# Kernel optimization log

Hardware: AMD Instinct MI355X
Metric: run time of the kernel (lower is better)

## Reference

```python
import jax, jax.numpy as jnp
import numpy as np

N = 100000
E = 1600000
IN_CH = 128
EDGE_CH = 16
HID = 128
OUT = 4
EPS = 1e-12  # F.normalize eps


def l2_normalize(x):
    # matches torch.nn.functional.normalize(x, p=2, dim=1)
    norm = jnp.sqrt(jnp.sum(x * x, axis=1, keepdims=True))
    return x / jnp.maximum(norm, EPS)


def sage_conv(x, row, col, edge_attr, W, b, n_nodes):
    # gather source node feats, concat edge feats: [E, in+edge]
    m = jnp.concatenate([x[row], edge_attr], axis=1)
    m = l2_normalize(m)
    # scatter-mean by destination node
    s = jax.ops.segment_sum(m, col, num_segments=n_nodes)
    cnt = jax.ops.segment_sum(jnp.ones((m.shape[0],), m.dtype), col, num_segments=n_nodes)
    agg = s / jnp.maximum(cnt, 1.0)[:, None]
    out = agg @ W + b
    return l2_normalize(out)


def setup_inputs() -> dict:
    key = jax.random.key(0)
    ks = jax.random.split(key, 7)
    x = jax.random.normal(ks[0], (N, IN_CH), dtype=jnp.float32)
    edge_index = jax.random.randint(ks[1], (2, E), 0, N, dtype=jnp.int64)
    edge_attr = jax.random.normal(ks[2], (E, EDGE_CH), dtype=jnp.float32)
    W1 = jax.random.normal(ks[3], (IN_CH + EDGE_CH, HID), dtype=jnp.float32) / np.sqrt(IN_CH + EDGE_CH)
    b1 = jnp.zeros((HID,), dtype=jnp.float32)
    W2 = jax.random.normal(ks[4], (HID + EDGE_CH, OUT), dtype=jnp.float32) / np.sqrt(HID + EDGE_CH)
    b2 = jnp.zeros((OUT,), dtype=jnp.float32)
    return {"x": x, "edge_index": edge_index, "edge_attr": edge_attr,
            "W1": W1, "b1": b1, "W2": W2, "b2": b2}


def reference(x, edge_index, edge_attr, W1, b1, W2, b2):
    row, col = edge_index[0], edge_index[1]
    h = sage_conv(x, row, col, edge_attr, W1, b1, N)
    h = jax.nn.relu(h)  # dropout is identity in eval mode
    h = sage_conv(h, row, col, edge_attr, W2, b2, N)
    return jax.nn.sigmoid(h)
```

## Files before the change

### kernel.cpp

```cpp
#include <hip/hip_runtime.h>
#include <hip/hip_fp16.h>
#include <math.h>

#define N_NODES 100000
#define N_EDGES 1600000
#define CHUNK 1024
#define NCHUNKS ((N_NODES + CHUNK - 1) / CHUNK)

union H8 { uint4 u; __half2 h[4]; };

__device__ __forceinline__ float red32(float v) {
    #pragma unroll
    for (int m = 16; m >= 1; m >>= 1) v += __shfl_xor(v, m, 64);
    return v;
}

__global__ __launch_bounds__(256) void prep_edges(
        const float* __restrict__ ea, const int* __restrict__ col,
        const float* __restrict__ W2,
        float* __restrict__ sqea, float4* __restrict__ pea,
        __half* __restrict__ eah, int* __restrict__ cnt) {
    __shared__ float w2e[64];
    int t = threadIdx.x;
    if (t < 64) w2e[t] = W2[128 * 4 + t];
    __syncthreads();
    int e = blockIdx.x * 256 + t;
    if (e >= N_EDGES) return;
    const float4* p = (const float4*)(ea + (size_t)e * 16);
    float4 q0 = p[0], q1 = p[1], q2 = p[2], q3 = p[3];
    float a[16] = {q0.x,q0.y,q0.z,q0.w, q1.x,q1.y,q1.z,q1.w,
                   q2.x,q2.y,q2.z,q2.w, q3.x,q3.y,q3.z,q3.w};
    float s = 0.f;
    float4 pv = make_float4(0.f, 0.f, 0.f, 0.f);
    #pragma unroll
    for (int k = 0; k < 16; ++k) {
        s += a[k] * a[k];
        pv.x += a[k] * w2e[k * 4 + 0];
        pv.y += a[k] * w2e[k * 4 + 1];
        pv.z += a[k] * w2e[k * 4 + 2];
        pv.w += a[k] * w2e[k * 4 + 3];
    }
    sqea[e] = s;
    pea[e] = pv;
    H8 u0, u1;
    u0.h[0] = __float22half2_rn(make_float2(q0.x, q0.y));
    u0.h[1] = __float22half2_rn(make_float2(q0.z, q0.w));
    u0.h[2] = __float22half2_rn(make_float2(q1.x, q1.y));
    u0.h[3] = __float22half2_rn(make_float2(q1.z, q1.w));
    u1.h[0] = __float22half2_rn(make_float2(q2.x, q2.y));
    u1.h[1] = __float22half2_rn(make_float2(q2.z, q2.w));
    u1.h[2] = __float22half2_rn(make_float2(q3.x, q3.y));
    u1.h[3] = __float22half2_rn(make_float2(q3.z, q3.w));
    uint4* dst = (uint4*)(eah + (size_t)e * 16);
    dst[0] = u0.u; dst[1] = u1.u;
    atomicAdd(&cnt[col[e]], 1);
}

__global__ void scan_part(const int* __restrict__ cnt, int* __restrict__ psum) {
    __shared__ int sd[CHUNK];
    int i = blockIdx.x * CHUNK + threadIdx.x;
    sd[threadIdx.x] = (i < N_NODES) ? cnt[i] : 0;
    __syncthreads();
    for (int s = CHUNK / 2; s > 0; s >>= 1) {
        if (threadIdx.x < s) sd[threadIdx.x] += sd[threadIdx.x + s];
        __syncthreads();
    }
    if (threadIdx.x == 0) psum[blockIdx.x] = sd[0];
}

__global__ void scan_top(const int* __restrict__ psum, int* __restrict__ coff,
                         int* __restrict__ off) {
    if (blockIdx.x == 0 && threadIdx.x == 0) {
        int run = 0;
        for (int i = 0; i < NCHUNKS; ++i) { coff[i] = run; run += psum[i]; }
        off[N_NODES] = N_EDGES;
    }
}

__global__ void scan_apply(const int* __restrict__ cnt, const int* __restrict__ coff,
                           int* __restrict__ off, int* __restrict__ head) {
    __shared__ int sd[CHUNK];
    int i = blockIdx.x * CHUNK + threadIdx.x;
    int v = (i < N_NODES) ? cnt[i] : 0;
    sd[threadIdx.x] = v;
    __syncthreads();
    for (int s = 1; s < CHUNK; s <<= 1) {
        int t = (threadIdx.x >= s) ? sd[threadIdx.x - s] : 0;
        __syncthreads();
        sd[threadIdx.x] += t;
        __syncthreads();
    }
    if (i < N_NODES) {
        int excl = coff[blockIdx.x] + sd[threadIdx.x] - v;
        off[i] = excl;
        head[i] = excl;
    }
}

__global__ __launch_bounds__(256) void scatter_e(
        const int* __restrict__ row, const int* __restrict__ col,
        const float* __restrict__ nx, const float* __restrict__ sqea,
        int* __restrict__ head, int4* __restrict__ csr4, int* __restrict__ epos) {
    int e = blockIdx.x * blockDim.x + threadIdx.x;
    if (e >= N_EDGES) return;
    int c = col[e];
    int r = row[e];
    float w1 = rsqrtf(fmaxf(nx[r] + sqea[e], 1e-24f));
    int p = atomicAdd(&head[c], 1);
    int4 mt; mt.x = r; mt.y = __float_as_int(w1); mt.z = e; mt.w = 0;
    csr4[p] = mt;
    epos[e] = p;
}

__global__ __launch_bounds__(256) void gemm_y1h(const float* __restrict__ x,
                                                const float* __restrict__ W1,
                                                __half* __restrict__ y1h,
                                                float* __restrict__ nx) {
    __shared__ float xs[64][129];
    int r0 = blockIdx.x * 64;
    int t = threadIdx.x;
    for (int i = t; i < 64 * 32; i += 256) {
        int rr = i >> 5, c4 = (i & 31) * 4;
        int gr = r0 + rr;
        float4 v = (gr < N_NODES) ? *(const float4*)(x + (size_t)gr * 128 + c4)
                                  : make_float4(0.f, 0.f, 0.f, 0.f);
        xs[rr][c4] = v.x; xs[rr][c4 + 1] = v.y; xs[rr][c4 + 2] = v.z; xs[rr][c4 + 3] = v.w;
    }
    __syncthreads();
    {
        int rr = t >> 2, q = t & 3;
        float s = 0.f;
        #pragma unroll
        for (int k = 0; k < 32; ++k) { float v = xs[rr][q * 32 + k]; s += v * v; }
        s += __shfl_xor(s, 1, 64);
        s += __shfl_xor(s, 2, 64);
        if (q == 0 && r0 + rr < N_NODES) nx[r0 + rr] = s;
    }
    int tx = t & 31, ty = t >> 5;
    float4 acc[8];
    #pragma unroll
    for (int i = 0; i < 8; ++i) acc[i] = make_float4(0.f, 0.f, 0.f, 0.f);
    #pragma unroll 4
    for (int k = 0; k < 128; ++k) {
        float4 wv = *(const float4*)(W1 + (size_t)k * 128 + tx * 4);
        #pragma unroll
        for (int i = 0; i < 8; ++i) {
            float xv = xs[ty * 8 + i][k];
            acc[i].x += xv * wv.x; acc[i].y += xv * wv.y;
            acc[i].z += xv * wv.z; acc[i].w += xv * wv.w;
        }
    }
    #pragma unroll
    for (int i = 0; i < 8; ++i) {
        int rr = r0 + ty * 8 + i;
        if (rr < N_NODES) {
            H8 pk;
            pk.h[0] = __float22half2_rn(make_float2(acc[i].x, acc[i].y));
            pk.h[1] = __float22half2_rn(make_float2(acc[i].z, acc[i].w));
            *(uint2*)(y1h + (size_t)rr * 128 + tx * 4) = make_uint2(pk.u.x, pk.u.y);
        }
    }
}

__global__ __launch_bounds__(256) void layer1(
        const __half* __restrict__ y1h, const __half* __restrict__ eah,
        const int4* __restrict__ csr4, const int* __restrict__ off,
        const float* __restrict__ W1, const float* __restrict__ b1,
        const float* __restrict__ W2, float* __restrict__ hn) {
    __shared__ int4  smeta[4][64];
    __shared__ float strans[4][144];
    int wv = threadIdx.x >> 6;
    int node = (blockIdx.x << 2) | wv;
    int lane = threadIdx.x & 63;
    if (node >= N_NODES) return;
    int s = off[node], e = off[node + 1];
    int deg = e - s;
    int m = (deg < 64) ? deg : 64;
    if (lane < m) smeta[wv][lane] = csr4[s + lane];
    asm volatile("s_waitcnt lgkmcnt(0)" ::: "memory");

    int e4 = lane >> 4;
    int c8 = lane & 15;
    float4 a0 = make_float4(0,0,0,0), a1 = a0;
    float4 ae0 = a0, ae1 = a0;

    #pragma unroll 2
    for (int t = 0; t < m; t += 4) {
        int idx = t + e4;
        bool val = idx < m;
        int4 mt = smeta[wv][val ? idx : 0];
        float w = val ? __int_as_float(mt.y) : 0.f;
        H8 pk; pk.u = *(const uint4*)(y1h + (size_t)mt.x * 128 + c8 * 8);
        float2 f0 = __half22float2(pk.h[0]);
        float2 f1 = __half22float2(pk.h[1]);
        float2 f2 = __half22float2(pk.h[2]);
        float2 f3 = __half22float2(pk.h[3]);
        a0.x += f0.x * w; a0.y += f0.y * w; a0.z += f1.x * w; a0.w += f1.y * w;
        a1.x += f2.x * w; a1.y += f2.y * w; a1.z += f3.x * w; a1.w += f3.y * w;
        if (c8 < 2) {
            H8 ek; ek.u = *(const uint4*)(eah + (size_t)mt.z * 16 + c8 * 8);
            float2 g0 = __half22float2(ek.h[0]);
            float2 g1 = __half22float2(ek.h[1]);
            float2 g2 = __half22float2(ek.h[2]);
            float2 g3 = __half22float2(ek.h[3]);
            ae0.x += g0.x * w; ae0.y += g0.y * w; ae0.z += g1.x * w; ae0.w += g1.y * w;
            ae1.x += g2.x * w; ae1.y += g2.y * w; ae1.z += g3.x * w; ae1.w += g3.y * w;
        }
    }
    for (int t = 64 + e4; t < deg; t += 4) {
        int4 mt = csr4[s + t];
        float w = __int_as_float(mt.y);
        H8 pk; pk.u = *(const uint4*)(y1h + (size_t)mt.x * 128 + c8 * 8);
        float2 f0 = __half22float2(pk.h[0]);
        float2 f1 = __half22float2(pk.h[1]);
        float2 f2 = __half22float2(pk.h[2]);
        float2 f3 = __half22float2(pk.h[3]);
        a0.x += f0.x * w; a0.y += f0.y * w; a0.z += f1.x * w; a0.w += f1.y * w;
        a1.x += f2.x * w; a1.y += f2.y * w; a1.z += f3.x * w; a1.w += f3.y * w;
        if (c8 < 2) {
            H8 ek; ek.u = *(const uint4*)(eah + (size_t)mt.z * 16 + c8 * 8);
            float2 g0 = __half22float2(ek.h[0]);
            float2 g1 = __half22float2(ek.h[1]);
            float2 g2 = __half22float2(ek.h[2]);
            float2 g3 = __half22float2(ek.h[3]);
            ae0.x += g0.x * w; ae0.y += g0.y * w; ae0.z += g1.x * w; ae0.w += g1.y * w;
            ae1.x += g2.x * w; ae1.y += g2.y * w; ae1.z += g3.x * w; ae1.w += g3.y * w;
        }
    }
    #pragma unroll
    for (int mm = 16; mm <= 32; mm <<= 1) {
        a0.x += __shfl_xor(a0.x, mm, 64); a0.y += __shfl_xor(a0.y, mm, 64);
        a0.z += __shfl_xor(a0.z, mm, 64); a0.w += __shfl_xor(a0.w, mm, 64);
        a1.x += __shfl_xor(a1.x, mm, 64); a1.y += __shfl_xor(a1.y, mm, 64);
        a1.z += __shfl_xor(a1.z, mm, 64); a1.w += __shfl_xor(a1.w, mm, 64);
        ae0.x += __shfl_xor(ae0.x, mm, 64); ae0.y += __shfl_xor(ae0.y, mm, 64);
        ae0.z += __shfl_xor(ae0.z, mm, 64); ae0.w += __shfl_xor(ae0.w, mm, 64);
        ae1.x += __shfl_xor(ae1.x, mm, 64); ae1.y += __shfl_xor(ae1.y, mm, 64);
        ae1.z += __shfl_xor(ae1.z, mm, 64); ae1.w += __shfl_xor(ae1.w, mm, 64);
    }
    if (e4 == 0) {
        *(float4*)&strans[wv][c8 * 8]     = a0;
        *(float4*)&strans[wv][c8 * 8 + 4] = a1;
        if (c8 < 2) {
            *(float4*)&strans[wv][128 + c8 * 8]     = ae0;
            *(float4*)&strans[wv][128 + c8 * 8 + 4] = ae1;
        }
    }
    asm volatile("s_waitcnt lgkmcnt(0)" ::: "memory");

    int c = lane & 31;
    float ic = 1.0f / fmaxf((float)deg, 1.0f);
    float4 av = *(const float4*)&strans[wv][c * 4];
    float4 b1v = *(const float4*)(b1 + c * 4);
    float4 o;
    o.x = av.x * ic + b1v.x; o.y = av.y * ic + b1v.y;
    o.z = av.z * ic + b1v.z; o.w = av.w * ic + b1v.w;
    #pragma unroll
    for (int k = 0; k < 16; ++k) {
        float sk = strans[wv][128 + k] * ic;
        float4 wv4 = *((const float4*)(W1 + (size_t)(128 + k) * 128) + c);
        o.x += sk * wv4.x; o.y += sk * wv4.y; o.z += sk * wv4.z; o.w += sk * wv4.w;
    }
    float ss    = o.x*o.x + o.y*o.y + o.z*o.z + o.w*o.w;
    float sspos = (o.x > 0.f ? o.x*o.x : 0.f) + (o.y > 0.f ? o.y*o.y : 0.f)
                + (o.z > 0.f ? o.z*o.z : 0.f) + (o.w > 0.f ? o.w*o.w : 0.f);
    ss = red32(ss);
    sspos = red32(sspos);
    float inv = rsqrtf(fmaxf(ss, 1e-24f));
    float4 h4;
    h4.x = fmaxf(o.x * inv, 0.f); h4.y = fmaxf(o.y * inv, 0.f);
    h4.z = fmaxf(o.z * inv, 0.f); h4.w = fmaxf(o.w * inv, 0.f);
    float nhv = sspos * inv * inv;
    float4 w0 = *(const float4*)(W2 + (size_t)(4*c + 0) * 4);
    float4 w1 = *(const float4*)(W2 + (size_t)(4*c + 1) * 4);
    float4 w2 = *(const float4*)(W2 + (size_t)(4*c + 2) * 4);
    float4 w3 = *(const float4*)(W2 + (size_t)(4*c + 3) * 4);
    float4 p;
    p.x = h4.x*w0.x + h4.y*w1.x + h4.z*w2.x + h4.w*w3.x;
    p.y = h4.x*w0.y + h4.y*w1.y + h4.z*w2.y + h4.w*w3.y;
    p.z = h4.x*w0.z + h4.y*w1.z + h4.z*w2.z + h4.w*w3.z;
    p.w = h4.x*w0.w + h4.y*w1.w + h4.z*w2.w + h4.w*w3.w;
    p.x = red32(p.x); p.y = red32(p.y); p.z = red32(p.z); p.w = red32(p.w);
    if (lane == 0) {
        *(float4*)(hn + (size_t)node * 8) = p;
        hn[(size_t)node * 8 + 4] = nhv;
    }
}

__global__ __launch_bounds__(256) void cpass(
        const int* __restrict__ row, const float* __restrict__ hn,
        const float* __restrict__ sqea, const float4* __restrict__ pea,
        const int* __restrict__ epos, float4* __restrict__ cbuf) {
    int e = blockIdx.x * blockDim.x + threadIdx.x;
    if (e >= N_EDGES) return;
    int r = row[e];
    float4 yh4 = *(const float4*)(hn + (size_t)r * 8);
    float nhr = hn[(size_t)r * 8 + 4];
    float w2 = rsqrtf(fmaxf(nhr + sqea[e], 1e-24f));
    float4 pe = pea[e];
    float4 cv;
    cv.x = (yh4.x + pe.x) * w2; cv.y = (yh4.y + pe.y) * w2;
    cv.z = (yh4.z + pe.z) * w2; cv.w = (yh4.w + pe.w) * w2;
    cbuf[epos[e]] = cv;
}

__global__ __launch_bounds__(256) void layer2b(
        const float4* __restrict__ cbuf, const int* __restrict__ off,
        const float* __restrict__ b2, float* __restrict__ out) {
    int v = blockIdx.x * blockDim.x + threadIdx.x;
    if (v >= N_NODES) return;
    int s = off[v], e = off[v + 1];
    float4 a = make_float4(0.f, 0.f, 0.f, 0.f);
    for (int t = s; t < e; ++t) {
        float4 cv = cbuf[t];
        a.x += cv.x; a.y += cv.y; a.z += cv.z; a.w += cv.w;
    }
    float ic = 1.0f / fmaxf((float)(e - s), 1.0f);
    float4 o;
    o.x = a.x * ic + b2[0]; o.y = a.y * ic + b2[1];
    o.z = a.z * ic + b2[2]; o.w = a.w * ic + b2[3];
    float ss = o.x*o.x + o.y*o.y + o.z*o.z + o.w*o.w;
    float inv = rsqrtf(fmaxf(ss, 1e-24f));
    float4 res;
    res.x = 1.0f / (1.0f + expf(-(o.x * inv)));
    res.y = 1.0f / (1.0f + expf(-(o.y * inv)));
    res.z = 1.0f / (1.0f + expf(-(o.z * inv)));
    res.w = 1.0f / (1.0f + expf(-(o.w * inv)));
    *(float4*)(out + (size_t)v * 4) = res;
}

extern "C" void kernel_launch(void* const* d_in, const int* in_sizes, int n_in,
                              void* d_out, int out_size, void* d_ws, size_t ws_size,
                              hipStream_t stream) {
    const float* x   = (const float*)d_in[0];
    const int*   ei  = (const int*)d_in[1];
    const float* ea  = (const float*)d_in[2];
    const float* W1  = (const float*)d_in[3];
    const float* b1  = (const float*)d_in[4];
    const float* W2  = (const float*)d_in[5];
    const float* b2  = (const float*)d_in[6];
    const int* row = ei;
    const int* col = ei + N_EDGES;
    float* out = (float*)d_out;

    char* ws = (char*)d_ws;
    size_t o = 0;
    auto carve = [&](size_t bytes) { char* p = ws + o; o = (o + bytes + 255) & ~(size_t)255; return p; };
    __half* y1h    = (__half*)carve((size_t)N_NODES * 128 * 2);
    float4* cbuf   = (float4*)y1h;
    float*  sqea   = (float*)carve((size_t)N_EDGES * 4);
    int4*   csr4   = (int4*)carve((size_t)N_EDGES * 16);
    int*    epos   = (int*)carve((size_t)N_EDGES * 4);
    float4* pea    = (float4*)carve((size_t)N_EDGES * 16);
    __half* eah    = (__half*)carve((size_t)N_EDGES * 16 * 2);
    int*    cnt    = (int*)carve((size_t)N_NODES * 4);
    int*    off    = (int*)carve((size_t)(N_NODES + 1) * 4);
    int*    head   = (int*)carve((size_t)N_NODES * 4);
    float*  nx     = (float*)carve((size_t)N_NODES * 4);
    float*  hn     = (float*)carve((size_t)N_NODES * 8 * 4);
    int*    psum   = (int*)carve((size_t)NCHUNKS * 4);
    int*    coff   = (int*)carve((size_t)NCHUNKS * 4);
    (void)ws_size; (void)in_sizes; (void)n_in; (void)out_size;

    hipMemsetAsync(cnt, 0, (size_t)N_NODES * 4, stream);

    dim3 b256(256);
    prep_edges<<<(N_EDGES + 255) / 256, b256, 0, stream>>>(ea, col, W2, sqea, pea, eah, cnt);
    gemm_y1h<<<(N_NODES + 63) / 64, b256, 0, stream>>>(x, W1, y1h, nx);

    scan_part<<<NCHUNKS, CHUNK, 0, stream>>>(cnt, psum);
    scan_top<<<1, 64, 0, stream>>>(psum, coff, off);
    scan_apply<<<NCHUNKS, CHUNK, 0, stream>>>(cnt, coff, off, head);
    scatter_e<<<(N_EDGES + 255) / 256, b256, 0, stream>>>(row, col, nx, sqea, head,
                                                          csr4, epos);

    layer1<<<(N_NODES + 3) / 4, b256, 0, stream>>>(y1h, eah, csr4, off, W1, b1, W2, hn);
    cpass<<<(N_EDGES + 255) / 256, b256, 0, stream>>>(row, hn, sqea, pea, epos, cbuf);
    layer2b<<<(N_NODES + 255) / 256, b256, 0, stream>>>(cbuf, off, b2, out);
}
```

Measured before the change: 427.8 us.

## Store edge data in CSR order and fuse layer-2 edge pass into node gather

Splits the histogram out of edge prep, then fuses edge preprocessing into the scatter kernel so that edge-feature halves, edge projections and squared norms are written directly at their CSR slot. Layer 1 then reads edge features contiguously instead of through an edge-id indirection, and the CSR metadata shrinks from 16 to 8 bytes. The separate cpass and layer2b kernels are replaced by a single wave-per-node layer2 kernel that computes each edge contribution and reduces it with shuffles, removing the cbuf round trip and the epos array. The cost is scattered writes of larger per-edge payloads during scatter_e, and one wave per node in layer2 leaves most lanes idle when degree is low.

```diff
diff --git a/kernel.cpp b/kernel.cpp
--- a/kernel.cpp
+++ b/kernel.cpp
@@ -15,11 +15,60 @@
     return v;
 }
 
-__global__ __launch_bounds__(256) void prep_edges(
-        const float* __restrict__ ea, const int* __restrict__ col,
-        const float* __restrict__ W2,
-        float* __restrict__ sqea, float4* __restrict__ pea,
-        __half* __restrict__ eah, int* __restrict__ cnt) {
+__global__ __launch_bounds__(256) void hist(const int* __restrict__ col,
+                                            int* __restrict__ cnt) {
+    int e = blockIdx.x * blockDim.x + threadIdx.x;
+    if (e >= N_EDGES) return;
+    atomicAdd(&cnt[col[e]], 1);
+}
+
+__global__ void scan_part(const int* __restrict__ cnt, int* __restrict__ psum) {
+    __shared__ int sd[CHUNK];
+    int i = blockIdx.x * CHUNK + threadIdx.x;
+    sd[threadIdx.x] = (i < N_NODES) ? cnt[i] : 0;
+    __syncthreads();
+    for (int s = CHUNK / 2; s > 0; s >>= 1) {
+        if (threadIdx.x < s) sd[threadIdx.x] += sd[threadIdx.x + s];
+        __syncthreads();
+    }
+    if (threadIdx.x == 0) psum[blockIdx.x] = sd[0];
+}
+
+__global__ void scan_top(const int* __restrict__ psum, int* __restrict__ coff,
+                         int* __restrict__ off) {
+    if (blockIdx.x == 0 && threadIdx.x == 0) {
+        int run = 0;
+        for (int i = 0; i < NCHUNKS; ++i) { coff[i] = run; run += psum[i]; }
+        off[N_NODES] = N_EDGES;
+    }
+}
+
+__global__ void scan_apply(const int* __restrict__ cnt, const int* __restrict__ coff,
+                           int* __restrict__ off, int* __restrict__ head) {
+    __shared__ int sd[CHUNK];
+    int i = blockIdx.x * CHUNK + threadIdx.x;
+    int v = (i < N_NODES) ? cnt[i] : 0;
+    sd[threadIdx.x] = v;
+    __syncthreads();
+    for (int s = 1; s < CHUNK; s <<= 1) {
+        int t = (threadIdx.x >= s) ? sd[threadIdx.x - s] : 0;
+        __syncthreads();
+        sd[threadIdx.x] += t;
+        __syncthreads();
+    }
+    if (i < N_NODES) {
+        int excl = coff[blockIdx.x] + sd[threadIdx.x] - v;
+        off[i] = excl;
+        head[i] = excl;
+    }
+}
+
+__global__ __launch_bounds__(256) void scatter_e(
+        const int* __restrict__ row, const int* __restrict__ col,
+        const float* __restrict__ nx, const float* __restrict__ ea,
+        const float* __restrict__ W2, int* __restrict__ head,
+        float2* __restrict__ csrA, float2* __restrict__ csrB,
+        float4* __restrict__ peaC, __half* __restrict__ eahC) {
     __shared__ float w2e[64];
     int t = threadIdx.x;
     if (t < 64) w2e[t] = W2[128 * 4 + t];
@@ -40,8 +89,13 @@
         pv.z += a[k] * w2e[k * 4 + 2];
         pv.w += a[k] * w2e[k * 4 + 3];
     }
-    sqea[e] = s;
-    pea[e] = pv;
+    int r = row[e];
+    int c = col[e];
+    float w1 = rsqrtf(fmaxf(nx[r] + s, 1e-24f));
+    int pp = atomicAdd(&head[c], 1);
+    csrA[pp] = make_float2(__int_as_float(r), w1);
+    csrB[pp] = make_float2(__int_as_float(r), s);
+    peaC[pp] = pv;
     H8 u0, u1;
     u0.h[0] = __float22half2_rn(make_float2(q0.x, q0.y));
     u0.h[1] = __float22half2_rn(make_float2(q0.z, q0.w));
@@ -51,65 +105,8 @@
     u1.h[1] = __float22half2_rn(make_float2(q2.z, q2.w));
     u1.h[2] = __float22half2_rn(make_float2(q3.x, q3.y));
     u1.h[3] = __float22half2_rn(make_float2(q3.z, q3.w));
-    uint4* dst = (uint4*)(eah + (size_t)e * 16);
+    uint4* dst = (uint4*)(eahC + (size_t)pp * 16);
     dst[0] = u0.u; dst[1] = u1.u;
-    atomicAdd(&cnt[col[e]], 1);
-}
-
-__global__ void scan_part(const int* __restrict__ cnt, int* __restrict__ psum) {
-    __shared__ int sd[CHUNK];
-    int i = blockIdx.x * CHUNK + threadIdx.x;
-    sd[threadIdx.x] = (i < N_NODES) ? cnt[i] : 0;
-    __syncthreads();
-    for (int s = CHUNK / 2; s > 0; s >>= 1) {
-        if (threadIdx.x < s) sd[threadIdx.x] += sd[threadIdx.x + s];
-        __syncthreads();
-    }
-    if (threadIdx.x == 0) psum[blockIdx.x] = sd[0];
-}
-
-__global__ void scan_top(const int* __restrict__ psum, int* __restrict__ coff,
-                         int* __restrict__ off) {
-    if (blockIdx.x == 0 && threadIdx.x == 0) {
-        int run = 0;
-        for (int i = 0; i < NCHUNKS; ++i) { coff[i] = run; run += psum[i]; }
-        off[N_NODES] = N_EDGES;
-    }
-}
-
-__global__ void scan_apply(const int* __restrict__ cnt, const int* __restrict__ coff,
-                           int* __restrict__ off, int* __restrict__ head) {
-    __shared__ int sd[CHUNK];
-    int i = blockIdx.x * CHUNK + threadIdx.x;
-    int v = (i < N_NODES) ? cnt[i] : 0;
-    sd[threadIdx.x] = v;
-    __syncthreads();
-    for (int s = 1; s < CHUNK; s <<= 1) {
-        int t = (threadIdx.x >= s) ? sd[threadIdx.x - s] : 0;
-        __syncthreads();
-        sd[threadIdx.x] += t;
-        __syncthreads();
-    }
-    if (i < N_NODES) {
-        int excl = coff[blockIdx.x] + sd[threadIdx.x] - v;
-        off[i] = excl;
-        head[i] = excl;
-    }
-}
-
-__global__ __launch_bounds__(256) void scatter_e(
-        const int* __restrict__ row, const int* __restrict__ col,
-        const float* __restrict__ nx, const float* __restrict__ sqea,
-        int* __restrict__ head, int4* __restrict__ csr4, int* __restrict__ epos) {
-    int e = blockIdx.x * blockDim.x + threadIdx.x;
-    if (e >= N_EDGES) return;
-    int c = col[e];
-    int r = row[e];
-    float w1 = rsqrtf(fmaxf(nx[r] + sqea[e], 1e-24f));
-    int p = atomicAdd(&head[c], 1);
-    int4 mt; mt.x = r; mt.y = __float_as_int(w1); mt.z = e; mt.w = 0;
-    csr4[p] = mt;
-    epos[e] = p;
 }
 
 __global__ __launch_bounds__(256) void gemm_y1h(const float* __restrict__ x,
@@ -163,11 +160,11 @@
 }
 
 __global__ __launch_bounds__(256) void layer1(
-        const __half* __restrict__ y1h, const __half* __restrict__ eah,
-        const int4* __restrict__ csr4, const int* __restrict__ off,
+        const __half* __restrict__ y1h, const __half* __restrict__ eahC,
+        const float2* __restrict__ csrA, const int* __restrict__ off,
         const float* __restrict__ W1, const float* __restrict__ b1,
         const float* __restrict__ W2, float* __restrict__ hn) {
-    __shared__ int4  smeta[4][64];
+    __shared__ float2 smeta[4][64];
     __shared__ float strans[4][144];
     int wv = threadIdx.x >> 6;
     int node = (blockIdx.x << 2) | wv;
@@ -176,7 +173,7 @@
     int s = off[node], e = off[node + 1];
     int deg = e - s;
     int m = (deg < 64) ? deg : 64;
-    if (lane < m) smeta[wv][lane] = csr4[s + lane];
+    if (lane < m) smeta[wv][lane] = csrA[s + lane];
     asm volatile("s_waitcnt lgkmcnt(0)" ::: "memory");
 
     int e4 = lane >> 4;
@@ -188,9 +185,10 @@
     for (int t = 0; t < m; t += 4) {
         int idx = t + e4;
         bool val = idx < m;
-        int4 mt = smeta[wv][val ? idx : 0];
-        float w = val ? __int_as_float(mt.y) : 0.f;
-        H8 pk; pk.u = *(const uint4*)(y1h + (size_t)mt.x * 128 + c8 * 8);
+        float2 mt = smeta[wv][val ? idx : 0];
+        int r = __float_as_int(mt.x);
+        float w = val ? mt.y : 0.f;
+        H8 pk; pk.u = *(const uint4*)(y1h + (size_t)r * 128 + c8 * 8);
         float2 f0 = __half22float2(pk.h[0]);
         float2 f1 = __half22float2(pk.h[1]);
         float2 f2 = __half22float2(pk.h[2]);
@@ -198,7 +196,7 @@
         a0.x += f0.x * w; a0.y += f0.y * w; a0.z += f1.x * w; a0.w += f1.y * w;
         a1.x += f2.x * w; a1.y += f2.y * w; a1.z += f3.x * w; a1.w += f3.y * w;
         if (c8 < 2) {
-            H8 ek; ek.u = *(const uint4*)(eah + (size_t)mt.z * 16 + c8 * 8);
+            H8 ek; ek.u = *(const uint4*)(eahC + (size_t)(s + idx) * 16 + c8 * 8);
             float2 g0 = __half22float2(ek.h[0]);
             float2 g1 = __half22float2(ek.h[1]);
             float2 g2 = __half22float2(ek.h[2]);
@@ -208,9 +206,10 @@
         }
     }
     for (int t = 64 + e4; t < deg; t += 4) {
-        int4 mt = csr4[s + t];
-        float w = __int_as_float(mt.y);
-        H8 pk; pk.u = *(const uint4*)(y1h + (size_t)mt.x * 128 + c8 * 8);
+        float2 mt = csrA[s + t];
+        int r = __float_as_int(mt.x);
+        float w = mt.y;
+        H8 pk; pk.u = *(const uint4*)(y1h + (size_t)r * 128 + c8 * 8);
         float2 f0 = __half22float2(pk.h[0]);
         float2 f1 = __half22float2(pk.h[1]);
         float2 f2 = __half22float2(pk.h[2]);
@@ -218,7 +217,7 @@
         a0.x += f0.x * w; a0.y += f0.y * w; a0.z += f1.x * w; a0.w += f1.y * w;
         a1.x += f2.x * w; a1.y += f2.y * w; a1.z += f3.x * w; a1.w += f3.y * w;
         if (c8 < 2) {
-            H8 ek; ek.u = *(const uint4*)(eah + (size_t)mt.z * 16 + c8 * 8);
+            H8 ek; ek.u = *(const uint4*)(eahC + (size_t)(s + t) * 16 + c8 * 8);
             float2 g0 = __half22float2(ek.h[0]);
             float2 g1 = __half22float2(ek.h[1]);
             float2 g2 = __half22float2(ek.h[2]);
@@ -287,46 +286,49 @@
     }
 }
 
-__global__ __launch_bounds__(256) void cpass(
-        const int* __restrict__ row, const float* __restrict__ hn,
-        const float* __restrict__ sqea, const float4* __restrict__ pea,
-        const int* __restrict__ epos, float4* __restrict__ cbuf) {
-    int e = blockIdx.x * blockDim.x + threadIdx.x;
-    if (e >= N_EDGES) return;
-    int r = row[e];
-    float4 yh4 = *(const float4*)(hn + (size_t)r * 8);
-    float nhr = hn[(size_t)r * 8 + 4];
-    float w2 = rsqrtf(fmaxf(nhr + sqea[e], 1e-24f));
-    float4 pe = pea[e];
-    float4 cv;
-    cv.x = (yh4.x + pe.x) * w2; cv.y = (yh4.y + pe.y) * w2;
-    cv.z = (yh4.z + pe.z) * w2; cv.w = (yh4.w + pe.w) * w2;
-    cbuf[epos[e]] = cv;
-}
-
-__global__ __launch_bounds__(256) void layer2b(
-        const float4* __restrict__ cbuf, const int* __restrict__ off,
+__global__ __launch_bounds__(256) void layer2(
+        const float2* __restrict__ csrB, const float4* __restrict__ peaC,
+        const float* __restrict__ hn, const int* __restrict__ off,
         const float* __restrict__ b2, float* __restrict__ out) {
-    int v = blockIdx.x * blockDim.x + threadIdx.x;
-    if (v >= N_NODES) return;
-    int s = off[v], e = off[v + 1];
-    float4 a = make_float4(0.f, 0.f, 0.f, 0.f);
-    for (int t = s; t < e; ++t) {
-        float4 cv = cbuf[t];
-        a.x += cv.x; a.y += cv.y; a.z += cv.z; a.w += cv.w;
-    }
-    float ic = 1.0f / fmaxf((float)(e - s), 1.0f);
-    float4 o;
-    o.x = a.x * ic + b2[0]; o.y = a.y * ic + b2[1];
-    o.z = a.z * ic + b2[2]; o.w = a.w * ic + b2[3];
-    float ss = o.x*o.x + o.y*o.y + o.z*o.z + o.w*o.w;
-    float inv = rsqrtf(fmaxf(ss, 1e-24f));
-    float4 res;
-    res.x = 1.0f / (1.0f + expf(-(o.x * inv)));
-    res.y = 1.0f / (1.0f + expf(-(o.y * inv)));
-    res.z = 1.0f / (1.0f + expf(-(o.z * inv)));
-    res.w = 1.0f / (1.0f + expf(-(o.w * inv)));
-    *(float4*)(out + (size_t)v * 4) = res;
+    int wv = threadIdx.x >> 6;
+    int node = (blockIdx.x << 2) | wv;
+    int lane = threadIdx.x & 63;
+    if (node >= N_NODES) return;
+    int s = off[node], e = off[node + 1];
+    int deg = e - s;
+    float4 acc = make_float4(0.f, 0.f, 0.f, 0.f);
+    for (int t = lane; t < deg; t += 64) {
+        float2 mb = csrB[s + t];
+        int r = __float_as_int(mb.x);
+        float sq = mb.y;
+        float4 yh = *(const float4*)(hn + (size_t)r * 8);
+        float nh = hn[(size_t)r * 8 + 4];
+        float w = rsqrtf(fmaxf(nh + sq, 1e-24f));
+        float4 pe = peaC[s + t];
+        acc.x += (yh.x + pe.x) * w; acc.y += (yh.y + pe.y) * w;
+        acc.z += (yh.z + pe.z) * w; acc.w += (yh.w + pe.w) * w;
+    }
+    #pragma unroll
+    for (int mm = 32; mm >= 1; mm >>= 1) {
+        acc.x += __shfl_xor(acc.x, mm, 64);
+        acc.y += __shfl_xor(acc.y, mm, 64);
+        acc.z += __shfl_xor(acc.z, mm, 64);
+        acc.w += __shfl_xor(acc.w, mm, 64);
+    }
+    if (lane == 0) {
+        float ic = 1.0f / fmaxf((float)deg, 1.0f);
+        float4 o;
+        o.x = acc.x * ic + b2[0]; o.y = acc.y * ic + b2[1];
+        o.z = acc.z * ic + b2[2]; o.w = acc.w * ic + b2[3];
+        float ss = o.x*o.x + o.y*o.y + o.z*o.z + o.w*o.w;
+        float inv = rsqrtf(fmaxf(ss, 1e-24f));
+        float4 res;
+        res.x = 1.0f / (1.0f + expf(-(o.x * inv)));
+        res.y = 1.0f / (1.0f + expf(-(o.y * inv)));
+        res.z = 1.0f / (1.0f + expf(-(o.z * inv)));
+        res.w = 1.0f / (1.0f + expf(-(o.w * inv)));
+        *(float4*)(out + (size_t)node * 4) = res;
+    }
 }
 
 extern "C" void kernel_launch(void* const* d_in, const int* in_sizes, int n_in,
@@ -347,12 +349,10 @@
     size_t o = 0;
     auto carve = [&](size_t bytes) { char* p = ws + o; o = (o + bytes + 255) & ~(size_t)255; return p; };
     __half* y1h    = (__half*)carve((size_t)N_NODES * 128 * 2);
-    float4* cbuf   = (float4*)y1h;
-    float*  sqea   = (float*)carve((size_t)N_EDGES * 4);
-    int4*   csr4   = (int4*)carve((size_t)N_EDGES * 16);
-    int*    epos   = (int*)carve((size_t)N_EDGES * 4);
-    float4* pea    = (float4*)carve((size_t)N_EDGES * 16);
-    __half* eah    = (__half*)carve((size_t)N_EDGES * 16 * 2);
+    float2* csrA   = (float2*)carve((size_t)N_EDGES * 8);
+    float2* csrB   = (float2*)carve((size_t)N_EDGES * 8);
+    float4* peaC   = (float4*)carve((size_t)N_EDGES * 16);
+    __half* eahC   = (__half*)carve((size_t)N_EDGES * 16 * 2);
     int*    cnt    = (int*)carve((size_t)N_NODES * 4);
     int*    off    = (int*)carve((size_t)(N_NODES + 1) * 4);
     int*    head   = (int*)carve((size_t)N_NODES * 4);
@@ -365,16 +365,15 @@
     hipMemsetAsync(cnt, 0, (size_t)N_NODES * 4, stream);
 
     dim3 b256(256);
-    prep_edges<<<(N_EDGES + 255) / 256, b256, 0, stream>>>(ea, col, W2, sqea, pea, eah, cnt);
+    hist<<<(N_EDGES + 255) / 256, b256, 0, stream>>>(col, cnt);
     gemm_y1h<<<(N_NODES + 63) / 64, b256, 0, stream>>>(x, W1, y1h, nx);
 
     scan_part<<<NCHUNKS, CHUNK, 0, stream>>>(cnt, psum);
     scan_top<<<1, 64, 0, stream>>>(psum, coff, off);
     scan_apply<<<NCHUNKS, CHUNK, 0, stream>>>(cnt, coff, off, head);
-    scatter_e<<<(N_EDGES + 255) / 256, b256, 0, stream>>>(row, col, nx, sqea, head,
-                                                          csr4, epos);
-
-    layer1<<<(N_NODES + 3) / 4, b256, 0, stream>>>(y1h, eah, csr4, off, W1, b1, W2, hn);
-    cpass<<<(N_EDGES + 255) / 256, b256, 0, stream>>>(row, hn, sqea, pea, epos, cbuf);
-    layer2b<<<(N_NODES + 255) / 256, b256, 0, stream>>>(cbuf, off, b2, out);
-}
+    scatter_e<<<(N_EDGES + 255) / 256, b256, 0, stream>>>(row, col, nx, ea, W2, head,
+                                                          csrA, csrB, peaC, eahC);
+
+    layer1<<<(N_NODES + 3) / 4, b256, 0, stream>>>(y1h, eahC, csrA, off, W1, b1, W2, hn);
+    layer2<<<(N_NODES + 3) / 4, b256, 0, stream>>>(csrB, peaC, hn, off, b2, out);
+}
```

Result: slower. 508.3 us (+18.8%).
